# Kernel tuning notes

Hardware: AMD Instinct MI355X
Metric: run time of the kernel (lower is better)

## Reference

```python
import jax, jax.numpy as jnp
import numpy as np

B, S, HID = 2, 2048, 2048
H, DH = 16, 128
SCALE = 1.0 / np.sqrt(DH)


def setup_inputs() -> dict:
    key = jax.random.key(0)
    ks = jax.random.split(key, 5)
    std = 1.0 / np.sqrt(HID)
    return {
        "x": jax.random.normal(ks[0], (B, S, HID), dtype=jnp.float32),
        "wq": jax.random.normal(ks[1], (HID, HID), dtype=jnp.float32) * std,
        "wk": jax.random.normal(ks[2], (HID, HID), dtype=jnp.float32) * std,
        "wv": jax.random.normal(ks[3], (HID, HID), dtype=jnp.float32) * std,
        "wo": jax.random.normal(ks[4], (HID, HID), dtype=jnp.float32) * std,
    }


def reference(x, wq, wk, wv, wo):
    # nn.Linear(h, h, bias=False): y = x @ W^T
    q = (x @ wq.T).reshape(B, S, H, DH).transpose(0, 2, 1, 3)  # [B,H,S,Dh]
    k = (x @ wk.T).reshape(B, S, H, DH).transpose(0, 2, 1, 3)
    v = (x @ wv.T).reshape(B, S, H, DH).transpose(0, 2, 1, 3)
    scores = jnp.einsum("bhsd,bhtd->bhst", q, k) * SCALE  # [B,H,S,S]
    attn = jax.nn.softmax(scores.astype(jnp.float32), axis=-1).astype(q.dtype)
    # dropout p=0.0 (eval): identity
    out = jnp.einsum("bhst,bhtd->bhsd", attn, v)  # [B,H,S,Dh]
    out = out.transpose(0, 2, 1, 3).reshape(B, S, HID)
    return out @ wo.T
```

## Files before the change

kernel.cpp:

```cpp
#include <hip/hip_runtime.h>
#include <hip/hip_bf16.h>
#include <stdint.h>

typedef __attribute__((ext_vector_type(8))) short short8;
typedef __attribute__((ext_vector_type(4))) float f32x4;
typedef __attribute__((ext_vector_type(4))) unsigned int uint4v;

static __device__ __forceinline__ ushort f2bf(float f) {
    uint32_t u = __builtin_bit_cast(uint32_t, f);
    uint32_t r = (u + 0x7FFFu + ((u >> 16) & 1u)) >> 16;
    return (ushort)r;
}

static __device__ __forceinline__ uint32_t cvt_pk_bf16(float lo, float hi) {
    uint32_t d;
    asm("v_cvt_pk_bf16_f32 %0, %1, %2" : "=v"(d) : "v"(lo), "v"(hi));
    return d;
}

static __device__ __forceinline__ void async_copy16(const void* g, void* l) {
    __builtin_amdgcn_global_load_lds(
        (const __attribute__((address_space(1))) uint32_t*)g,
        (__attribute__((address_space(3))) uint32_t*)l, 16, 0, 0);
}

__global__ __launch_bounds__(256) void cast_kernel(const float* __restrict__ in,
                                                   ushort* __restrict__ out, int n4) {
    int i = blockIdx.x * 256 + threadIdx.x;
    if (i >= n4) return;
    float4 v = reinterpret_cast<const float4*>(in)[i];
    uint2 o;
    o.x = cvt_pk_bf16(v.x, v.y);
    o.y = cvt_pk_bf16(v.z, v.w);
    reinterpret_cast<uint2*>(out)[i] = o;
}

__global__ __launch_bounds__(256) void cast3_kernel(const float* __restrict__ a,
                                                    const float* __restrict__ b,
                                                    const float* __restrict__ c,
                                                    ushort* __restrict__ out, int n4each) {
    int i = blockIdx.x * 256 + threadIdx.x;
    int which = i / n4each;
    int j = i - which * n4each;
    const float* src = which == 0 ? a : (which == 1 ? b : c);
    if (which > 2) return;
    float4 v = reinterpret_cast<const float4*>(src)[j];
    uint2 o;
    o.x = cvt_pk_bf16(v.x, v.y);
    o.y = cvt_pk_bf16(v.z, v.w);
    reinterpret_cast<uint2*>(out)[i] = o;
}

static __device__ __forceinline__ void store_val(float* C, size_t idx, float v) { C[idx] = v; }
static __device__ __forceinline__ void store_val(ushort* C, size_t idx, float v) { C[idx] = f2bf(v); }

template <typename OutT>
__global__ __launch_bounds__(256) void gemm_bt_kernel(const ushort* __restrict__ A,
                                                      const ushort* __restrict__ B,
                                                      OutT* __restrict__ C,
                                                      int M, int N, int K) {
    __shared__ __align__(16) ushort As[128 * 32];
    __shared__ __align__(16) ushort Bs[128 * 32];
    const int tid = threadIdx.x;
    const int w = tid >> 6, lane = tid & 63;
    const int fr = lane & 15, fq = lane >> 4;
    const int wr = w >> 1, wc = w & 1;
    const int bpn = N >> 7;
    const int which = blockIdx.x / bpn;
    const int row0 = blockIdx.y * 128;
    const int gcol0 = blockIdx.x * 128;
    const int col0 = gcol0 - which * N;
    OutT* Cw = C + (size_t)which * M * N;

    const int srow = tid >> 2;
    const int scol = (tid & 3) * 8;
    const ushort* ga0 = A + (size_t)(row0 + srow) * K + scol;
    const ushort* ga1 = A + (size_t)(row0 + 64 + srow) * K + scol;
    const ushort* gb0 = B + (size_t)(gcol0 + srow) * K + scol;
    const ushort* gb1 = B + (size_t)(gcol0 + 64 + srow) * K + scol;
    ushort* la0 = &As[(w * 64) * 8];
    ushort* la1 = &As[(256 + w * 64) * 8];
    ushort* lb0 = &Bs[(w * 64) * 8];
    ushort* lb1 = &Bs[(256 + w * 64) * 8];

    f32x4 acc[4][4];
#pragma unroll
    for (int m = 0; m < 4; ++m)
#pragma unroll
        for (int n = 0; n < 4; ++n) acc[m][n] = f32x4{0.f, 0.f, 0.f, 0.f};

    for (int kt = 0; kt < K; kt += 32) {
        __syncthreads();
        async_copy16(ga0 + kt, la0);
        async_copy16(ga1 + kt, la1);
        async_copy16(gb0 + kt, lb0);
        async_copy16(gb1 + kt, lb1);
        __syncthreads();
        short8 af[4], bfr[4];
#pragma unroll
        for (int m = 0; m < 4; ++m)
            af[m] = *(const short8*)&As[(wr * 64 + m * 16 + fr) * 32 + fq * 8];
#pragma unroll
        for (int n = 0; n < 4; ++n)
            bfr[n] = *(const short8*)&Bs[(wc * 64 + n * 16 + fr) * 32 + fq * 8];
#pragma unroll
        for (int m = 0; m < 4; ++m)
#pragma unroll
            for (int n = 0; n < 4; ++n)
                acc[m][n] = __builtin_amdgcn_mfma_f32_16x16x32_bf16(af[m], bfr[n], acc[m][n], 0, 0, 0);
    }

#pragma unroll
    for (int m = 0; m < 4; ++m) {
        const int grow = row0 + wr * 64 + m * 16 + fq * 4;
#pragma unroll
        for (int n = 0; n < 4; ++n) {
            const int gcol = col0 + wc * 64 + n * 16 + fr;
#pragma unroll
            for (int r = 0; r < 4; ++r)
                store_val(Cw, (size_t)(grow + r) * N + gcol, acc[m][n][r]);
        }
    }
}

__global__ __launch_bounds__(512, 2) void gemm256_kernel(const ushort* __restrict__ A,
                                                         const ushort* __restrict__ B,
                                                         ushort* __restrict__ C,
                                                         int M, int N, int K) {
    __shared__ __align__(16) char smem[131072];
    const int tid = threadIdx.x, w = tid >> 6, lane = tid & 63;
    const int fr = lane & 15, fq = lane >> 4;
    const int wm = w >> 2, wn = w & 3;
    const int bpn = N >> 8;
    const int which = blockIdx.x / bpn;
    const int row0 = blockIdx.y * 256;
    const int gcol0 = blockIdx.x * 256;
    const int col0 = gcol0 - which * N;
    ushort* Cw = C + (size_t)which * M * N;

    const int lo = ((tid & 7) ^ ((tid >> 3) & 7)) << 4;
    const int r0p = ((tid >> 3) << 1) + (lo >> 6);
    const int colE = (lo & 63) >> 1;
    const ushort* Ap0 = A + (size_t)(row0 + r0p) * K + colE;
    const ushort* Ap1 = A + (size_t)(row0 + 128 + r0p) * K + colE;
    const ushort* Bp0 = B + (size_t)(gcol0 + r0p) * K + colE;
    const ushort* Bp1 = B + (size_t)(gcol0 + 128 + r0p) * K + colE;

    char* aregs = smem;
    char* bregs = smem + 65536;
    const int wbyte = w * 1024;

    auto stageH = [&](int h) {
        const int kc = (h >> 1) * 64 + (h & 1) * 32;
        char* ar = aregs + (h & 3) * 16384;
        char* br = bregs + (h & 3) * 16384;
        async_copy16(Ap0 + kc, ar + wbyte);
        async_copy16(Ap1 + kc, ar + 8192 + wbyte);
        async_copy16(Bp0 + kc, br + wbyte);
        async_copy16(Bp1 + kc, br + 8192 + wbyte);
    };

    const int swz = ((fr & 1) * 64 + fq * 16) ^ (((fr >> 1) & 7) << 4);
    const int aBase = (wm * 64 + (fr >> 1)) * 128 + swz;
    const int bBase = (wn * 32 + (fr >> 1)) * 128 + swz;

    f32x4 acc[8][4];
#pragma unroll
    for (int m = 0; m < 8; ++m)
#pragma unroll
        for (int n = 0; n < 4; ++n) acc[m][n] = f32x4{0.f, 0.f, 0.f, 0.f};

    const int nH = K >> 5;
    stageH(0); stageH(1); stageH(2);
    asm volatile("s_waitcnt vmcnt(8)\n\ts_barrier" ::: "memory");

    for (int i = 0; i < nH; ++i) {
        if (i + 3 < nH) stageH(i + 3);
        const char* ar = aregs + (i & 3) * 16384 + aBase;
        const char* br = bregs + (i & 3) * 16384 + bBase;
        short8 af[8], bf[4];
#pragma unroll
        for (int m = 0; m < 8; ++m) af[m] = *(const short8*)(ar + m * 1024);
#pragma unroll
        for (int n = 0; n < 4; ++n) bf[n] = *(const short8*)(br + n * 1024);
        __builtin_amdgcn_s_setprio(1);
#pragma unroll
        for (int m = 0; m < 8; ++m)
#pragma unroll
            for (int n = 0; n < 4; ++n)
                acc[m][n] = __builtin_amdgcn_mfma_f32_16x16x32_bf16(af[m], bf[n], acc[m][n], 0, 0, 0);
        __builtin_amdgcn_s_setprio(0);
        if (i < nH - 3)
            asm volatile("s_waitcnt vmcnt(8)\n\ts_barrier" ::: "memory");
        else if (i == nH - 3)
            asm volatile("s_waitcnt vmcnt(4)\n\ts_barrier" ::: "memory");
        else if (i == nH - 2)
            asm volatile("s_waitcnt vmcnt(0)\n\ts_barrier" ::: "memory");
    }

#pragma unroll
    for (int m = 0; m < 8; ++m) {
        const int grow = row0 + wm * 128 + m * 16 + fq * 4;
#pragma unroll
        for (int n = 0; n < 4; ++n) {
            const int gcol = col0 + wn * 64 + n * 16 + fr;
#pragma unroll
            for (int r2 = 0; r2 < 4; ++r2)
                Cw[(size_t)(grow + r2) * N + gcol] = f2bf(acc[m][n][r2]);
        }
    }
}

__global__ __launch_bounds__(512) void attn_kernel(const ushort* __restrict__ Q,
                                                   const ushort* __restrict__ K,
                                                   const ushort* __restrict__ VT,
                                                   ushort* __restrict__ O,
                                                   int S, int HID, float scale) {
    __shared__ __align__(16) ushort Ks[2][64 * 128];
    __shared__ __align__(16) ushort Vts[2][128 * 64];

    const int tid = threadIdx.x, w = tid >> 6, lane = tid & 63;
    const int fr = lane & 15, fq = lane >> 4;
    const int h = blockIdx.x & 15, b = blockIdx.x >> 4, qt = blockIdx.y;
    const size_t rs = (size_t)HID;
    const size_t vs = (size_t)(2 * S);
    const int qr0 = qt * 128 + w * 16;
    const float c1 = scale * 1.4426950408889634f;

    short8 qf[4];
    {
        const ushort* qp = Q + ((size_t)(b * S) + qr0 + fr) * rs + h * 128 + fq * 8;
#pragma unroll
        for (int ks = 0; ks < 4; ++ks) qf[ks] = *(const short8*)(qp + ks * 32);
    }

    f32x4 of[8];
#pragma unroll
    for (int n = 0; n < 8; ++n) of[n] = f32x4{0.f, 0.f, 0.f, 0.f};
    float m2 = -1e30f;
    float l = 0.f;

    const ushort* Kb = K + (size_t)(b * S) * rs + h * 128;
    const ushort* Vb = VT + (size_t)(h * 128) * vs + b * S;

    size_t koff[2];
#pragma unroll
    for (int j = 0; j < 2; ++j) {
        int row = j * 32 + w * 4 + (lane >> 4);
        int colb = ((lane & 15) * 16) ^ ((row & 7) << 4);
        koff[j] = (size_t)row * rs + (colb >> 1);
    }
    size_t vtoff[2];
#pragma unroll
    for (int j = 0; j < 2; ++j) {
        int row = j * 64 + (tid >> 3);
        int colb = ((tid & 7) * 16) ^ ((row & 7) << 4);
        vtoff[j] = (size_t)row * vs + (colb >> 1);
    }

    auto stage = [&](int t) {
        const int bufb = t & 1;
        const ushort* kt0 = Kb + (size_t)t * 64 * rs;
        const ushort* vt0 = Vb + (size_t)t * 64;
#pragma unroll
        for (int j = 0; j < 2; ++j)
            async_copy16(kt0 + koff[j], &Ks[bufb][j * 4096 + w * 512]);
#pragma unroll
        for (int j = 0; j < 2; ++j)
            async_copy16(vt0 + vtoff[j], &Vts[bufb][j * 4096 + w * 512]);
    };

    const int srcA = fr + 16 * ((2 * fq) & 3);
    const int srcB = fr + 16 * ((2 * fq + 1) & 3);
    const int par = fq >> 1;

    const int nt = S / 64;
    stage(0);
    for (int t = 0; t < nt; ++t) {
        __builtin_amdgcn_s_barrier();
        __builtin_amdgcn_sched_barrier(0);
        if (t + 1 < nt) {
            stage(t + 1);
            asm volatile("s_waitcnt vmcnt(4)" ::: "memory");
        } else {
            asm volatile("s_waitcnt vmcnt(0)" ::: "memory");
        }
        __builtin_amdgcn_s_barrier();
        __builtin_amdgcn_sched_barrier(0);

        const char* kbase = (const char*)&Ks[t & 1][0];
        const char* vbase = (const char*)&Vts[t & 1][0];

        f32x4 sf[4];
        __builtin_amdgcn_s_setprio(1);
#pragma unroll
        for (int kc = 0; kc < 4; ++kc) {
            f32x4 s = f32x4{0.f, 0.f, 0.f, 0.f};
#pragma unroll
            for (int ks = 0; ks < 4; ++ks) {
                int row = kc * 16 + fr;
                int pb = (row * 256 + ks * 64 + fq * 16) ^ ((row & 7) << 4);
                short8 kf = *(const short8*)(kbase + pb);
                s = __builtin_amdgcn_mfma_f32_16x16x32_bf16(kf, qf[ks], s, 0, 0, 0);
            }
            sf[kc] = s;
        }
        __builtin_amdgcn_s_setprio(0);

        float pm = fmaxf(fmaxf(fmaxf(sf[0][0], sf[0][1]), fmaxf(sf[0][2], sf[0][3])),
                         fmaxf(fmaxf(sf[1][0], sf[1][1]), fmaxf(sf[1][2], sf[1][3])));
        pm = fmaxf(pm, fmaxf(fmaxf(fmaxf(sf[2][0], sf[2][1]), fmaxf(sf[2][2], sf[2][3])),
                             fmaxf(fmaxf(sf[3][0], sf[3][1]), fmaxf(sf[3][2], sf[3][3]))));
        pm = fmaxf(pm, __shfl_xor(pm, 16));
        pm = fmaxf(pm, __shfl_xor(pm, 32));
        float pm2 = pm * c1;
        const bool noresc = __all(pm2 - m2 <= 8.0f);
        float sc = 1.0f;
        if (!noresc) {
            float m2new = fmaxf(m2, pm2);
            sc = exp2f(m2 - m2new);
            m2 = m2new;
        }
        float rsum = 0.f;
#pragma unroll
        for (int kc = 0; kc < 4; ++kc)
#pragma unroll
            for (int r = 0; r < 4; ++r) {
                float p = exp2f(sf[kc][r] * c1 - m2);
                sf[kc][r] = p;
                rsum += p;
            }
        rsum += __shfl_xor(rsum, 16);
        rsum += __shfl_xor(rsum, 32);
        if (noresc) {
            l = l + rsum;
        } else {
            l = l * sc + rsum;
#pragma unroll
            for (int n = 0; n < 8; ++n) {
                f32x4 o = of[n];
                o[0] *= sc; o[1] *= sc; o[2] *= sc; o[3] *= sc;
                of[n] = o;
            }
        }

        uint32_t cpk[4][2];
#pragma unroll
        for (int kc = 0; kc < 4; ++kc)
#pragma unroll
            for (int hh = 0; hh < 2; ++hh)
                cpk[kc][hh] = cvt_pk_bf16(sf[kc][2 * hh], sf[kc][2 * hh + 1]);

        __builtin_amdgcn_s_setprio(1);
#pragma unroll
        for (int kvc = 0; kvc < 2; ++kvc) {
            uint32_t eA0 = __shfl(cpk[2 * kvc][0], srcA), eA1 = __shfl(cpk[2 * kvc][1], srcA);
            uint32_t oA0 = __shfl(cpk[2 * kvc + 1][0], srcA), oA1 = __shfl(cpk[2 * kvc + 1][1], srcA);
            uint32_t eB0 = __shfl(cpk[2 * kvc][0], srcB), eB1 = __shfl(cpk[2 * kvc][1], srcB);
            uint32_t oB0 = __shfl(cpk[2 * kvc + 1][0], srcB), oB1 = __shfl(cpk[2 * kvc + 1][1], srcB);
            uint4v pd;
            pd[0] = par ? oA0 : eA0; pd[1] = par ? oA1 : eA1;
            pd[2] = par ? oB0 : eB0; pd[3] = par ? oB1 : eB1;
            short8 pf = __builtin_bit_cast(short8, pd);
#pragma unroll
            for (int n = 0; n < 8; ++n) {
                int row = n * 16 + fr;
                int pb = row * 128 + ((kvc * 64 + fq * 16) ^ ((row & 7) << 4));
                short8 vf = *(const short8*)(vbase + pb);
                of[n] = __builtin_amdgcn_mfma_f32_16x16x32_bf16(vf, pf, of[n], 0, 0, 0);
            }
        }
        __builtin_amdgcn_s_setprio(0);
    }

    float inv = 1.f / l;
    ushort* ob = O + ((size_t)(b * S) + qr0 + fr) * rs + h * 128 + fq * 4;
#pragma unroll
    for (int n = 0; n < 8; ++n) {
        uint2 o2;
        o2.x = cvt_pk_bf16(of[n][0] * inv, of[n][1] * inv);
        o2.y = cvt_pk_bf16(of[n][2] * inv, of[n][3] * inv);
        *reinterpret_cast<uint2*>(ob + n * 16) = o2;
    }
}

extern "C" void kernel_launch(void* const* d_in, const int* in_sizes, int n_in,
                              void* d_out, int out_size, void* d_ws, size_t ws_size,
                              hipStream_t stream) {
    constexpr int B = 2, S = 2048, HID = 2048, H = 16;
    constexpr int M = B * S;
    const float scale = 0.08838834764831845f;

    const float* x  = (const float*)d_in[0];
    const float* wq = (const float*)d_in[1];
    const float* wk = (const float*)d_in[2];
    const float* wv = (const float*)d_in[3];
    const float* wo = (const float*)d_in[4];
    float* out = (float*)d_out;

    char* ws = (char*)d_ws;
    ushort* xb  = (ushort*)(ws);
    ushort* wqb = (ushort*)(ws + 16777216);
    ushort* wvb = (ushort*)(ws + 33554432);
    ushort* qb  = (ushort*)(ws + 41943040);
    ushort* kb  = (ushort*)(ws + 58720256);
    ushort* vtb = (ushort*)(ws + 75497472);

    const int XN = M * HID;
    const int WN = HID * HID;

    cast_kernel<<<XN / 4 / 256, 256, 0, stream>>>(x, xb, XN / 4);
    cast3_kernel<<<3 * WN / 4 / 256, 256, 0, stream>>>(wq, wk, wv, wqb, WN / 4);

    dim3 gq(2 * HID / 256, M / 256);
    gemm256_kernel<<<gq, 512, 0, stream>>>(xb, wqb, qb, M, HID, HID);

    dim3 gv(M / 128, HID / 128);
    gemm_bt_kernel<ushort><<<gv, 256, 0, stream>>>(wvb, xb, vtb, HID, M, HID);

    dim3 ga(H * B, S / 128);
    attn_kernel<<<ga, 512, 0, stream>>>(qb, kb, vtb, xb, S, HID, scale);

    cast_kernel<<<WN / 4 / 256, 256, 0, stream>>>(wo, wqb, WN / 4);
    dim3 gg(HID / 128, M / 128);
    gemm_bt_kernel<float><<<gg, 256, 0, stream>>>(xb, wqb, out, M, HID, HID);
}
```

Measured before the change: 323.1 us.

## Process two 16-row query tiles per wave in attention to reuse K/V fragments

Each wave now handles 32 query rows (two 16-row subtiles) instead of 16, so every K and V fragment read from LDS feeds two MFMAs. The query tile per block doubles to 256 and the grid's y dimension halves. This cuts LDS reads and global K/V staging per query row. In exchange it roughly doubles accumulator and score register use, which may lower occupancy or cause spills. The grid shrinks to 256 blocks, which may underfill the GPU's compute units.

```diff
diff --git a/kernel.cpp b/kernel.cpp
--- a/kernel.cpp
+++ b/kernel.cpp
@@ -224,21 +224,24 @@
     const int h = blockIdx.x & 15, b = blockIdx.x >> 4, qt = blockIdx.y;
     const size_t rs = (size_t)HID;
     const size_t vs = (size_t)(2 * S);
-    const int qr0 = qt * 128 + w * 16;
+    const int qr0 = qt * 256 + w * 32;
     const float c1 = scale * 1.4426950408889634f;
 
-    short8 qf[4];
-    {
-        const ushort* qp = Q + ((size_t)(b * S) + qr0 + fr) * rs + h * 128 + fq * 8;
-#pragma unroll
-        for (int ks = 0; ks < 4; ++ks) qf[ks] = *(const short8*)(qp + ks * 32);
-    }
-
-    f32x4 of[8];
-#pragma unroll
-    for (int n = 0; n < 8; ++n) of[n] = f32x4{0.f, 0.f, 0.f, 0.f};
-    float m2 = -1e30f;
-    float l = 0.f;
+    short8 qf[2][4];
+#pragma unroll
+    for (int qh = 0; qh < 2; ++qh) {
+        const ushort* qp = Q + ((size_t)(b * S) + qr0 + qh * 16 + fr) * rs + h * 128 + fq * 8;
+#pragma unroll
+        for (int ks = 0; ks < 4; ++ks) qf[qh][ks] = *(const short8*)(qp + ks * 32);
+    }
+
+    f32x4 of[2][8];
+#pragma unroll
+    for (int qh = 0; qh < 2; ++qh)
+#pragma unroll
+        for (int n = 0; n < 8; ++n) of[qh][n] = f32x4{0.f, 0.f, 0.f, 0.f};
+    float m2[2] = {-1e30f, -1e30f};
+    float l[2] = {0.f, 0.f};
 
     const ushort* Kb = K + (size_t)(b * S) * rs + h * 128;
     const ushort* Vb = VT + (size_t)(h * 128) * vs + b * S;
@@ -291,96 +294,109 @@
         const char* kbase = (const char*)&Ks[t & 1][0];
         const char* vbase = (const char*)&Vts[t & 1][0];
 
-        f32x4 sf[4];
+        f32x4 sf[2][4];
         __builtin_amdgcn_s_setprio(1);
 #pragma unroll
         for (int kc = 0; kc < 4; ++kc) {
-            f32x4 s = f32x4{0.f, 0.f, 0.f, 0.f};
+            f32x4 s0 = f32x4{0.f, 0.f, 0.f, 0.f};
+            f32x4 s1 = f32x4{0.f, 0.f, 0.f, 0.f};
 #pragma unroll
             for (int ks = 0; ks < 4; ++ks) {
                 int row = kc * 16 + fr;
                 int pb = (row * 256 + ks * 64 + fq * 16) ^ ((row & 7) << 4);
                 short8 kf = *(const short8*)(kbase + pb);
-                s = __builtin_amdgcn_mfma_f32_16x16x32_bf16(kf, qf[ks], s, 0, 0, 0);
+                s0 = __builtin_amdgcn_mfma_f32_16x16x32_bf16(kf, qf[0][ks], s0, 0, 0, 0);
+                s1 = __builtin_amdgcn_mfma_f32_16x16x32_bf16(kf, qf[1][ks], s1, 0, 0, 0);
             }
-            sf[kc] = s;
+            sf[0][kc] = s0;
+            sf[1][kc] = s1;
         }
         __builtin_amdgcn_s_setprio(0);
 
-        float pm = fmaxf(fmaxf(fmaxf(sf[0][0], sf[0][1]), fmaxf(sf[0][2], sf[0][3])),
-                         fmaxf(fmaxf(sf[1][0], sf[1][1]), fmaxf(sf[1][2], sf[1][3])));
-        pm = fmaxf(pm, fmaxf(fmaxf(fmaxf(sf[2][0], sf[2][1]), fmaxf(sf[2][2], sf[2][3])),
-                             fmaxf(fmaxf(sf[3][0], sf[3][1]), fmaxf(sf[3][2], sf[3][3]))));
-        pm = fmaxf(pm, __shfl_xor(pm, 16));
-        pm = fmaxf(pm, __shfl_xor(pm, 32));
-        float pm2 = pm * c1;
-        const bool noresc = __all(pm2 - m2 <= 8.0f);
-        float sc = 1.0f;
-        if (!noresc) {
-            float m2new = fmaxf(m2, pm2);
-            sc = exp2f(m2 - m2new);
-            m2 = m2new;
-        }
-        float rsum = 0.f;
-#pragma unroll
-        for (int kc = 0; kc < 4; ++kc)
-#pragma unroll
-            for (int r = 0; r < 4; ++r) {
-                float p = exp2f(sf[kc][r] * c1 - m2);
-                sf[kc][r] = p;
-                rsum += p;
+        uint32_t cpk[2][4][2];
+#pragma unroll
+        for (int qh = 0; qh < 2; ++qh) {
+            float pm = fmaxf(fmaxf(fmaxf(sf[qh][0][0], sf[qh][0][1]), fmaxf(sf[qh][0][2], sf[qh][0][3])),
+                             fmaxf(fmaxf(sf[qh][1][0], sf[qh][1][1]), fmaxf(sf[qh][1][2], sf[qh][1][3])));
+            pm = fmaxf(pm, fmaxf(fmaxf(fmaxf(sf[qh][2][0], sf[qh][2][1]), fmaxf(sf[qh][2][2], sf[qh][2][3])),
+                                 fmaxf(fmaxf(sf[qh][3][0], sf[qh][3][1]), fmaxf(sf[qh][3][2], sf[qh][3][3]))));
+            pm = fmaxf(pm, __shfl_xor(pm, 16));
+            pm = fmaxf(pm, __shfl_xor(pm, 32));
+            float pm2 = pm * c1;
+            const bool noresc = __all(pm2 - m2[qh] <= 8.0f);
+            float sc = 1.0f;
+            if (!noresc) {
+                float m2new = fmaxf(m2[qh], pm2);
+                sc = exp2f(m2[qh] - m2new);
+                m2[qh] = m2new;
             }
-        rsum += __shfl_xor(rsum, 16);
-        rsum += __shfl_xor(rsum, 32);
-        if (noresc) {
-            l = l + rsum;
-        } else {
-            l = l * sc + rsum;
-#pragma unroll
-            for (int n = 0; n < 8; ++n) {
-                f32x4 o = of[n];
-                o[0] *= sc; o[1] *= sc; o[2] *= sc; o[3] *= sc;
-                of[n] = o;
+            float rsum = 0.f;
+#pragma unroll
+            for (int kc = 0; kc < 4; ++kc)
+#pragma unroll
+                for (int r = 0; r < 4; ++r) {
+                    float p = exp2f(sf[qh][kc][r] * c1 - m2[qh]);
+                    sf[qh][kc][r] = p;
+                    rsum += p;
+                }
+            rsum += __shfl_xor(rsum, 16);
+            rsum += __shfl_xor(rsum, 32);
+            if (noresc) {
+                l[qh] = l[qh] + rsum;
+            } else {
+                l[qh] = l[qh] * sc + rsum;
+#pragma unroll
+                for (int n = 0; n < 8; ++n) {
+                    f32x4 o = of[qh][n];
+                    o[0] *= sc; o[1] *= sc; o[2] *= sc; o[3] *= sc;
+                    of[qh][n] = o;
+                }
             }
-        }
-
-        uint32_t cpk[4][2];
-#pragma unroll
-        for (int kc = 0; kc < 4; ++kc)
-#pragma unroll
-            for (int hh = 0; hh < 2; ++hh)
-                cpk[kc][hh] = cvt_pk_bf16(sf[kc][2 * hh], sf[kc][2 * hh + 1]);
+#pragma unroll
+            for (int kc = 0; kc < 4; ++kc)
+#pragma unroll
+                for (int hh = 0; hh < 2; ++hh)
+                    cpk[qh][kc][hh] = cvt_pk_bf16(sf[qh][kc][2 * hh], sf[qh][kc][2 * hh + 1]);
+        }
 
         __builtin_amdgcn_s_setprio(1);
 #pragma unroll
         for (int kvc = 0; kvc < 2; ++kvc) {
-            uint32_t eA0 = __shfl(cpk[2 * kvc][0], srcA), eA1 = __shfl(cpk[2 * kvc][1], srcA);
-            uint32_t oA0 = __shfl(cpk[2 * kvc + 1][0], srcA), oA1 = __shfl(cpk[2 * kvc + 1][1], srcA);
-            uint32_t eB0 = __shfl(cpk[2 * kvc][0], srcB), eB1 = __shfl(cpk[2 * kvc][1], srcB);
-            uint32_t oB0 = __shfl(cpk[2 * kvc + 1][0], srcB), oB1 = __shfl(cpk[2 * kvc + 1][1], srcB);
-            uint4v pd;
-            pd[0] = par ? oA0 : eA0; pd[1] = par ? oA1 : eA1;
-            pd[2] = par ? oB0 : eB0; pd[3] = par ? oB1 : eB1;
-            short8 pf = __builtin_bit_cast(short8, pd);
+            short8 pf[2];
+#pragma unroll
+            for (int qh = 0; qh < 2; ++qh) {
+                uint32_t eA0 = __shfl(cpk[qh][2 * kvc][0], srcA), eA1 = __shfl(cpk[qh][2 * kvc][1], srcA);
+                uint32_t oA0 = __shfl(cpk[qh][2 * kvc + 1][0], srcA), oA1 = __shfl(cpk[qh][2 * kvc + 1][1], srcA);
+                uint32_t eB0 = __shfl(cpk[qh][2 * kvc][0], srcB), eB1 = __shfl(cpk[qh][2 * kvc][1], srcB);
+                uint32_t oB0 = __shfl(cpk[qh][2 * kvc + 1][0], srcB), oB1 = __shfl(cpk[qh][2 * kvc + 1][1], srcB);
+                uint4v pd;
+                pd[0] = par ? oA0 : eA0; pd[1] = par ? oA1 : eA1;
+                pd[2] = par ? oB0 : eB0; pd[3] = par ? oB1 : eB1;
+                pf[qh] = __builtin_bit_cast(short8, pd);
+            }
 #pragma unroll
             for (int n = 0; n < 8; ++n) {
                 int row = n * 16 + fr;
                 int pb = row * 128 + ((kvc * 64 + fq * 16) ^ ((row & 7) << 4));
                 short8 vf = *(const short8*)(vbase + pb);
-                of[n] = __builtin_amdgcn_mfma_f32_16x16x32_bf16(vf, pf, of[n], 0, 0, 0);
+                of[0][n] = __builtin_amdgcn_mfma_f32_16x16x32_bf16(vf, pf[0], of[0][n], 0, 0, 0);
+                of[1][n] = __builtin_amdgcn_mfma_f32_16x16x32_bf16(vf, pf[1], of[1][n], 0, 0, 0);
             }
         }
         __builtin_amdgcn_s_setprio(0);
     }
 
-    float inv = 1.f / l;
-    ushort* ob = O + ((size_t)(b * S) + qr0 + fr) * rs + h * 128 + fq * 4;
-#pragma unroll
-    for (int n = 0; n < 8; ++n) {
-        uint2 o2;
-        o2.x = cvt_pk_bf16(of[n][0] * inv, of[n][1] * inv);
-        o2.y = cvt_pk_bf16(of[n][2] * inv, of[n][3] * inv);
-        *reinterpret_cast<uint2*>(ob + n * 16) = o2;
+#pragma unroll
+    for (int qh = 0; qh < 2; ++qh) {
+        float inv = 1.f / l[qh];
+        ushort* ob = O + ((size_t)(b * S) + qr0 + qh * 16 + fr) * rs + h * 128 + fq * 4;
+#pragma unroll
+        for (int n = 0; n < 8; ++n) {
+            uint2 o2;
+            o2.x = cvt_pk_bf16(of[qh][n][0] * inv, of[qh][n][1] * inv);
+            o2.y = cvt_pk_bf16(of[qh][n][2] * inv, of[qh][n][3] * inv);
+            *reinterpret_cast<uint2*>(ob + n * 16) = o2;
+        }
     }
 }
 
@@ -418,7 +434,7 @@
     dim3 gv(M / 128, HID / 128);
     gemm_bt_kernel<ushort><<<gv, 256, 0, stream>>>(wvb, xb, vtb, HID, M, HID);
 
-    dim3 ga(H * B, S / 128);
+    dim3 ga(H * B, S / 256);
     attn_kernel<<<ga, 512, 0, stream>>>(qb, kb, vtb, xb, S, HID, scale);
 
     cast_kernel<<<WN / 4 / 256, 256, 0, stream>>>(wo, wqb, WN / 4);
```

After: 326.3 us. About the same (+1.0%).
